# Performance work log

Hardware: AMD Instinct MI355X
Metric: run time of the kernel (lower is better)

## Reference

```python
import jax, jax.numpy as jnp
import numpy as np

T, B, K = 512, 512, 8
V, H, NL, NLAB = 5, 30, 4, 3


def setup_inputs() -> dict:
    key = jax.random.key(0)
    ks = jax.random.split(key, 12)
    s = 0.1
    return {
        "x": jax.random.randint(ks[0], (T, B, K), 0, V),
        "weight_of_x": jax.random.uniform(ks[1], (T, B, K), dtype=jnp.float32),
        "embed": jax.random.normal(ks[2], (V, H), dtype=jnp.float32) * s,
        "lstm_Wih": jax.random.normal(ks[3], (NL, 4 * H, H), dtype=jnp.float32) * s,
        "lstm_Whh": jax.random.normal(ks[4], (NL, 4 * H, H), dtype=jnp.float32) * s,
        "lstm_bih": jax.random.normal(ks[5], (NL, 4 * H), dtype=jnp.float32) * s,
        "lstm_bhh": jax.random.normal(ks[6], (NL, 4 * H), dtype=jnp.float32) * s,
        "attn_W1": jax.random.normal(ks[7], (H, 64), dtype=jnp.float32) * s,
        "attn_b1": jnp.zeros((64,), jnp.float32),
        "attn_W2": jax.random.normal(ks[8], (64, 1), dtype=jnp.float32) * s,
        "attn_b2": jnp.zeros((1,), jnp.float32),
        "fc_W": jax.random.normal(ks[9], (H, NLAB), dtype=jnp.float32) * s,
        "fc_b": jnp.zeros((NLAB,), jnp.float32),
    }


def _lstm_layer(xs, Wih, Whh, bih, bhh):
    # xs: (T, B, H_in); PyTorch gate order i, f, g, o
    b = bih + bhh
    Bsz = xs.shape[1]
    h0 = jnp.zeros((Bsz, Whh.shape[1]), xs.dtype)

    def step(carry, xt):
        h, c = carry
        gates = xt @ Wih.T + h @ Whh.T + b  # (B, 4H)
        i, f, g, o = jnp.split(gates, 4, axis=-1)
        i, f, o = jax.nn.sigmoid(i), jax.nn.sigmoid(f), jax.nn.sigmoid(o)
        g = jnp.tanh(g)
        c = f * c + i * g
        h = o * jnp.tanh(c)
        return (h, c), h

    _, hs = jax.lax.scan(step, (h0, h0), xs)
    return hs  # (T, B, H)


def reference(x, weight_of_x, embed, lstm_Wih, lstm_Whh, lstm_bih, lstm_bhh,
              attn_W1, attn_b1, attn_W2, attn_b2, fc_W, fc_b):
    # embedding + weighted mean pooling over K
    e = embed[x] * weight_of_x[..., None]          # (T, B, K, H)
    e = jax.nn.relu(e)
    seq = jnp.mean(e, axis=2)                      # (T, B, H)

    # 4-layer LSTM (loop over fixed num_layers)
    out = seq
    for l in range(lstm_Wih.shape[0]):
        out = _lstm_layer(out, lstm_Wih[l], lstm_Whh[l], lstm_bih[l], lstm_bhh[l])

    # attention pooling over time
    enc = jnp.transpose(out, (1, 0, 2))            # (B, T, H)
    energy = jax.nn.relu(enc @ attn_W1 + attn_b1) @ attn_W2 + attn_b2  # (B, T, 1)
    weights = jax.nn.softmax(energy[..., 0], axis=1)  # (B, T)
    pooled = jnp.sum(enc * weights[..., None], axis=1)  # (B, H)

    # dropout is identity in eval mode
    logit = jax.nn.softmax(pooled @ fc_W + fc_b, axis=1)  # (B, 3)
    return logit
```

## Files before the change

### kernel.cpp

```cpp
#include <hip/hip_runtime.h>

#define TT 512
#define BB 512
#define KK 8
#define HH 30
#define GG 120
#define NLAYER 4

__device__ __forceinline__ float rcp_f(float x) { return __builtin_amdgcn_rcpf(x); }
__device__ __forceinline__ float rdlane_f(float v, int l) {
    return __int_as_float(__builtin_amdgcn_readlane(__float_as_int(v), l));
}
__device__ __forceinline__ float2 pk_fma_v(float2 a, float2 b, float2 c) {
    float2 d;
    asm("v_pk_fma_f32 %0, %1, %2, %3" : "=v"(d) : "v"(a), "v"(b), "v"(c));
    return d;
}
__device__ __forceinline__ float2 pk_fma_s(float2 a, float2 bs, float2 c) {
    float2 d;
    asm("v_pk_fma_f32 %0, %1, %2, %3" : "=v"(d) : "v"(a), "s"(bs), "v"(c));
    return d;
}
__device__ __forceinline__ float2 pk_add(float2 a, float2 b) {
    float2 d;
    asm("v_pk_add_f32 %0, %1, %2" : "=v"(d) : "v"(a), "v"(b));
    return d;
}
__device__ __forceinline__ float swap32_hi(float x) {
    float a = x, b = x;
    asm("v_permlane32_swap_b32 %0, %1" : "+v"(a), "+v"(b));
    return b;
}

__global__ __launch_bounds__(256) __attribute__((amdgpu_waves_per_eu(2, 2)))
void rnn_fused(
    const int*   __restrict__ xin,  const float* __restrict__ wxin,
    const float* __restrict__ embed,
    const float* __restrict__ Wih,  const float* __restrict__ Whh,
    const float* __restrict__ bih,  const float* __restrict__ bhh,
    const float* __restrict__ W1,   const float* __restrict__ b1,
    const float* __restrict__ W2,   const float* __restrict__ b2,
    const float* __restrict__ fcW,  const float* __restrict__ fcb,
    float* __restrict__ out)
{
    __shared__ alignas(16) float hstore[TT * HH];
    __shared__ alignas(16) float seqring[2][16][32];
    __shared__ alignas(16) int   ringx[4][16][KK];
    __shared__ alignas(16) float ringw[4][16][KK];
    __shared__ alignas(16) float hring[3][16][32];
    __shared__ alignas(16) float re_s[5 * HH];
    __shared__ alignas(16) float energy_s[TT];
    __shared__ float red_s[16];
    __shared__ float part_s[8][HH];
    __shared__ float pooled_s[HH];
    __shared__ float logits_s[3];
    __shared__ int   sync_s[8];

    const int tid  = threadIdx.x;
    const int wv   = tid >> 6;
    const int lane = tid & 63;
    const int b    = blockIdx.x;
    volatile int* vs = sync_s;

    if (tid < 8) sync_s[tid] = 0;
    if (tid < 5 * HH) re_s[tid] = fmaxf(embed[tid], 0.0f);

    int4 hx = {0,0,0,0}; float4 hw = {0,0,0,0};
    if (wv == 0 && lane < 32) {
        const int r = lane >> 1, hf = lane & 1;
        #pragma unroll
        for (int cc = 0; cc < 2; ++cc) {
            long off = ((long)(16 * cc + r) * BB + b) * KK + hf * 4;
            *(int4*)(&ringx[cc][r][hf * 4])   = *(const int4*)(xin  + off);
            *(float4*)(&ringw[cc][r][hf * 4]) = *(const float4*)(wxin + off);
        }
        long off2 = ((long)(32 + r) * BB + b) * KK + hf * 4;
        hx = *(const int4*)(xin  + off2);
        hw = *(const float4*)(wxin + off2);
    }

    const int half = lane >> 5;
    const int q31  = lane & 31;
    const int qq   = (q31 < HH) ? q31 : (HH - 1);
    const int rA   = qq + half * HH;
    const int rB   = rA + 60;
    float2 wihA[15], wihB[15], whhA[15], whhB[15];
    {
        const float* WihL = Wih + wv * GG * HH;
        const float* WhhL = Whh + wv * GG * HH;
        #pragma unroll
        for (int kk = 0; kk < 15; ++kk) {
            wihA[kk] = *(const float2*)(WihL + rA * HH + 2 * kk);
            wihB[kk] = *(const float2*)(WihL + rB * HH + 2 * kk);
            whhA[kk] = *(const float2*)(WhhL + rA * HH + 2 * kk);
            whhB[kk] = *(const float2*)(WhhL + rB * HH + 2 * kk);
        }
    }
    const float biasA = bih[wv * GG + rA] + bhh[wv * GG + rA];
    const float biasB = bih[wv * GG + rB] + bhh[wv * GG + rB];
    const float mBneg = (lane < 32) ? -2.0f : -1.0f;
    const float aB    = (lane < 32) ?  2.0f :  1.0f;
    const float dB    = (lane < 32) ? -1.0f :  0.0f;

    __syncthreads();

    float c_val = 0.0f;
    float hprev = 0.0f;

    auto do_step = [&](int t) {
        const float* xsrc = (wv == 0) ? &seqring[(t >> 4) & 1][t & 15][0]
                                      : &hring[wv - 1][t & 15][0];
        float2 xp[15];
        #pragma unroll
        for (int k = 0; k < 15; ++k) xp[k] = *(const float2*)(xsrc + 2 * k);

        float2 ahA = {0.f,0.f}, ahB = {0.f,0.f};
        float2 ahA2 = {0.f,0.f}, ahB2 = {0.f,0.f};
        #pragma unroll
        for (int k = 0; k < 8; ++k) {
            float2 hp;
            hp.x = rdlane_f(hprev, 2 * k);
            hp.y = rdlane_f(hprev, 2 * k + 1);
            ahA = pk_fma_s(whhA[k], hp, ahA);
            ahB = pk_fma_s(whhB[k], hp, ahB);
        }
        #pragma unroll
        for (int k = 8; k < 15; ++k) {
            float2 hp;
            hp.x = rdlane_f(hprev, 2 * k);
            hp.y = rdlane_f(hprev, 2 * k + 1);
            ahA2 = pk_fma_s(whhA[k], hp, ahA2);
            ahB2 = pk_fma_s(whhB[k], hp, ahB2);
        }
        float2 axA = {0.f,0.f}, axB = {0.f,0.f};
        #pragma unroll
        for (int k = 0; k < 15; ++k) {
            axA = pk_fma_v(wihA[k], xp[k], axA);
            axB = pk_fma_v(wihB[k], xp[k], axB);
        }
        const float2 s0 = pk_add(pk_add(axA, ahA), ahA2);
        const float2 s1 = pk_add(pk_add(axB, ahB), ahB2);
        const float gA = s0.x + s0.y + biasA;
        const float gB = s1.x + s1.y + biasB;
        const float actA = rcp_f(1.0f + __expf(-gA));
        const float sB   = rcp_f(1.0f + __expf(gB * mBneg));
        const float actB = fmaf(aB, sB, dB);
        const float fI = swap32_hi(actA);
        const float oI = swap32_hi(actB);
        c_val = fmaf(fI, c_val, actA * actB);
        const float tC = fmaf(2.0f, rcp_f(1.0f + __expf(-2.0f * c_val)), -1.0f);
        const float hv = oI * tC;
        hprev = hv;
        if (lane < HH) {
            if (wv < NLAYER - 1) hring[wv][t & 15][lane] = hv;
            else                 hstore[t * HH + lane]  = hv;
        }
    };

    for (int T0 = 0; T0 < TT; T0 += 8) {
        if (wv == 0) {
            if ((T0 & 15) == 0) {
                const int c = T0 >> 4;
                if (lane < 32) {
                    const int r = lane >> 1, hf = lane & 1;
                    if (c <= 29) {
                        const int sl = (c + 2) & 3;
                        *(int4*)(&ringx[sl][r][hf * 4])   = hx;
                        *(float4*)(&ringw[sl][r][hf * 4]) = hw;
                    }
                    if (c <= 28) {
                        long off = ((long)(16 * (c + 3) + r) * BB + b) * KK + hf * 4;
                        hx = *(const int4*)(xin  + off);
                        hw = *(const float4*)(wxin + off);
                    }
                }
                const int sl = c & 3, par = c & 1;
                #pragma unroll
                for (int rr = 0; rr < 8; ++rr) {
                    const int o = lane + rr * 64;
                    if (o < 480) {
                        const int tr = o / HH, j = o - tr * HH;
                        int4   xa = *(const int4*)(&ringx[sl][tr][0]);
                        int4   xb = *(const int4*)(&ringx[sl][tr][4]);
                        float4 wa = *(const float4*)(&ringw[sl][tr][0]);
                        float4 wb = *(const float4*)(&ringw[sl][tr][4]);
                        float acc = re_s[xa.x * HH + j] * wa.x;
                        acc = fmaf(re_s[xa.y * HH + j], wa.y, acc);
                        acc = fmaf(re_s[xa.z * HH + j], wa.z, acc);
                        acc = fmaf(re_s[xa.w * HH + j], wa.w, acc);
                        acc = fmaf(re_s[xb.x * HH + j], wb.x, acc);
                        acc = fmaf(re_s[xb.y * HH + j], wb.y, acc);
                        acc = fmaf(re_s[xb.z * HH + j], wb.z, acc);
                        acc = fmaf(re_s[xb.w * HH + j], wb.w, acc);
                        seqring[par][tr][j] = acc * 0.125f;
                    }
                }
                __threadfence_block();
            }
        } else {
            while (vs[wv - 1] < T0 + 8) __builtin_amdgcn_s_sleep(1);
        }
        if (wv < NLAYER - 1) {
            while (vs[4 + wv + 1] < T0 - 8) __builtin_amdgcn_s_sleep(1);
        }
        __threadfence_block();
        do_step(T0 + 0);
        do_step(T0 + 1);
        do_step(T0 + 2);
        do_step(T0 + 3);
        do_step(T0 + 4);
        do_step(T0 + 5);
        do_step(T0 + 6);
        do_step(T0 + 7);
        __threadfence_block();
        if (lane == 0) {
            if (wv < NLAYER - 1) vs[wv]     = T0 + 8;
            if (wv > 0)          vs[4 + wv] = T0 + 8;
        }
    }

    __syncthreads();

    {
        const float* W1p = W1;
        const float* b1p = b1;
        const float* W2p = W2;
        asm volatile("" : "+v"(W1p), "+v"(b1p), "+v"(W2p));

        float w1cx[15], w1cy[15];
        #pragma unroll
        for (int k = 0; k < 15; ++k) {
            w1cx[k] = W1p[(2 * k) * 64 + lane];
            w1cy[k] = W1p[(2 * k + 1) * 64 + lane];
        }
        const float b1v = b1p[lane];
        const float w2v = W2p[lane];
        const float b2v = b2[0];
        #pragma unroll
        for (int pass = 0; pass < 2; ++pass) {
            const int t = wv * 128 + pass * 64 + lane;
            float2 h2[15];
            #pragma unroll
            for (int k = 0; k < 15; ++k)
                h2[k] = *(const float2*)(hstore + t * HH + 2 * k);
            float e = b2v;
            for (int u = 0; u < 64; ++u) {
                float2 acc = {0.f, 0.f};
                #pragma unroll
                for (int k = 0; k < 15; ++k) {
                    float2 wp;
                    wp.x = rdlane_f(w1cx[k], u);
                    wp.y = rdlane_f(w1cy[k], u);
                    acc = pk_fma_s(h2[k], wp, acc);
                }
                const float su = acc.x + acc.y + rdlane_f(b1v, u);
                e = fmaf(fmaxf(su, 0.0f), rdlane_f(w2v, u), e);
            }
            energy_s[t] = e;
        }
    }
    __syncthreads();

    float mx = -3.0e38f;
    for (int i = tid; i < TT; i += 256) mx = fmaxf(mx, energy_s[i]);
    #pragma unroll
    for (int m = 1; m < 64; m <<= 1) mx = fmaxf(mx, __shfl_xor(mx, m, 64));
    if (lane == 0) red_s[wv] = mx;
    __syncthreads();
    mx = fmaxf(fmaxf(red_s[0], red_s[1]), fmaxf(red_s[2], red_s[3]));
    float ssum = 0.0f;
    for (int i = tid; i < TT; i += 256) {
        float ev = __expf(energy_s[i] - mx);
        energy_s[i] = ev;
        ssum += ev;
    }
    #pragma unroll
    for (int m = 1; m < 64; m <<= 1) ssum += __shfl_xor(ssum, m, 64);
    if (lane == 0) red_s[8 + wv] = ssum;
    __syncthreads();
    const float invS = rcp_f(red_s[8] + red_s[9] + red_s[10] + red_s[11]);

    {
        const int g = tid >> 5, jj = tid & 31;
        if (jj < HH) {
            float part = 0.0f;
            for (int t = g; t < TT; t += 8)
                part = fmaf(energy_s[t] * invS, hstore[t * HH + jj], part);
            part_s[g][jj] = part;
        }
    }
    __syncthreads();
    if (tid < HH) {
        float pv = 0.0f;
        #pragma unroll
        for (int q = 0; q < 8; ++q) pv += part_s[q][tid];
        pooled_s[tid] = pv;
    }
    __syncthreads();

    if (tid < 3) {
        float acc = fcb[tid];
        #pragma unroll
        for (int k = 0; k < HH; ++k) acc = fmaf(pooled_s[k], fcW[k * 3 + tid], acc);
        logits_s[tid] = acc;
    }
    __syncthreads();
    if (tid == 0) {
        float l0 = logits_s[0], l1 = logits_s[1], l2 = logits_s[2];
        float m3 = fmaxf(l0, fmaxf(l1, l2));
        float e0 = __expf(l0 - m3), e1 = __expf(l1 - m3), e2 = __expf(l2 - m3);
        float inv = rcp_f(e0 + e1 + e2);
        out[b * 3 + 0] = e0 * inv; out[b * 3 + 1] = e1 * inv; out[b * 3 + 2] = e2 * inv;
    }
}

extern "C" void kernel_launch(void* const* d_in, const int* in_sizes, int n_in,
                              void* d_out, int out_size, void* d_ws, size_t ws_size,
                              hipStream_t stream)
{
    (void)in_sizes; (void)n_in; (void)d_ws; (void)ws_size; (void)out_size;
    rnn_fused<<<BB, 256, 0, stream>>>(
        (const int*)  d_in[0],  (const float*)d_in[1],  (const float*)d_in[2],
        (const float*)d_in[3],  (const float*)d_in[4],  (const float*)d_in[5],
        (const float*)d_in[6],  (const float*)d_in[7],  (const float*)d_in[8],
        (const float*)d_in[9],  (const float*)d_in[10], (const float*)d_in[11],
        (const float*)d_in[12], (float*)d_out);
}
```

Before: 452.8 us.

## Use fp16 weights and activations with fdot2 in LSTM recurrence

Converts the LSTM input and recurrent weights to packed fp16 and accumulates the gate dot products with v_dot2 fp16 instructions into fp32. Inter-layer hidden states and the embedded sequence are stored as packed half2 in shared memory, and adjacent lanes' h values are combined with a DPP swap so one readlane fetches two h values. This halves the register footprint and the readlane count on the serial per-step critical path. It also stops unrolling the 8-step loop. The cost is fp16 rounding of weights and activations across 512 recurrent steps and 4 layers, which may exceed the accuracy tolerance.

```diff
diff --git a/kernel.cpp b/kernel.cpp
--- a/kernel.cpp
+++ b/kernel.cpp
@@ -7,23 +7,21 @@
 #define GG 120
 #define NLAYER 4
 
+typedef _Float16 half2v __attribute__((ext_vector_type(2)));
+
 __device__ __forceinline__ float rcp_f(float x) { return __builtin_amdgcn_rcpf(x); }
 __device__ __forceinline__ float rdlane_f(float v, int l) {
     return __int_as_float(__builtin_amdgcn_readlane(__float_as_int(v), l));
 }
-__device__ __forceinline__ float2 pk_fma_v(float2 a, float2 b, float2 c) {
-    float2 d;
-    asm("v_pk_fma_f32 %0, %1, %2, %3" : "=v"(d) : "v"(a), "v"(b), "v"(c));
-    return d;
+__device__ __forceinline__ unsigned int rdlane_u(unsigned int v, int l) {
+    return (unsigned int)__builtin_amdgcn_readlane((int)v, l);
+}
+__device__ __forceinline__ half2v as_h2(unsigned int u) {
+    union { unsigned int u; half2v h; } c; c.u = u; return c.h;
 }
 __device__ __forceinline__ float2 pk_fma_s(float2 a, float2 bs, float2 c) {
     float2 d;
     asm("v_pk_fma_f32 %0, %1, %2, %3" : "=v"(d) : "v"(a), "s"(bs), "v"(c));
-    return d;
-}
-__device__ __forceinline__ float2 pk_add(float2 a, float2 b) {
-    float2 d;
-    asm("v_pk_add_f32 %0, %1, %2" : "=v"(d) : "v"(a), "v"(b));
     return d;
 }
 __device__ __forceinline__ float swap32_hi(float x) {
@@ -44,10 +42,10 @@
     float* __restrict__ out)
 {
     __shared__ alignas(16) float hstore[TT * HH];
-    __shared__ alignas(16) float seqring[2][16][32];
+    __shared__ alignas(16) unsigned int seqring16[2][16][16];
     __shared__ alignas(16) int   ringx[4][16][KK];
     __shared__ alignas(16) float ringw[4][16][KK];
-    __shared__ alignas(16) float hring[3][16][32];
+    __shared__ alignas(16) unsigned int hring16[3][16][16];
     __shared__ alignas(16) float re_s[5 * HH];
     __shared__ alignas(16) float energy_s[TT];
     __shared__ float red_s[16];
@@ -84,16 +82,20 @@
     const int qq   = (q31 < HH) ? q31 : (HH - 1);
     const int rA   = qq + half * HH;
     const int rB   = rA + 60;
-    float2 wihA[15], wihB[15], whhA[15], whhB[15];
+    half2v wihA_h[15], wihB_h[15], whhA_h[15], whhB_h[15];
     {
         const float* WihL = Wih + wv * GG * HH;
         const float* WhhL = Whh + wv * GG * HH;
         #pragma unroll
         for (int kk = 0; kk < 15; ++kk) {
-            wihA[kk] = *(const float2*)(WihL + rA * HH + 2 * kk);
-            wihB[kk] = *(const float2*)(WihL + rB * HH + 2 * kk);
-            whhA[kk] = *(const float2*)(WhhL + rA * HH + 2 * kk);
-            whhB[kk] = *(const float2*)(WhhL + rB * HH + 2 * kk);
+            float2 a0 = *(const float2*)(WihL + rA * HH + 2 * kk);
+            float2 a1 = *(const float2*)(WihL + rB * HH + 2 * kk);
+            float2 a2 = *(const float2*)(WhhL + rA * HH + 2 * kk);
+            float2 a3 = *(const float2*)(WhhL + rB * HH + 2 * kk);
+            wihA_h[kk][0] = (_Float16)a0.x; wihA_h[kk][1] = (_Float16)a0.y;
+            wihB_h[kk][0] = (_Float16)a1.x; wihB_h[kk][1] = (_Float16)a1.y;
+            whhA_h[kk][0] = (_Float16)a2.x; whhA_h[kk][1] = (_Float16)a2.y;
+            whhB_h[kk][0] = (_Float16)a3.x; whhB_h[kk][1] = (_Float16)a3.y;
         }
     }
     const float biasA = bih[wv * GG + rA] + bhh[wv * GG + rA];
@@ -105,43 +107,39 @@
     __syncthreads();
 
     float c_val = 0.0f;
-    float hprev = 0.0f;
+    unsigned int hpk = 0;
 
     auto do_step = [&](int t) {
-        const float* xsrc = (wv == 0) ? &seqring[(t >> 4) & 1][t & 15][0]
-                                      : &hring[wv - 1][t & 15][0];
-        float2 xp[15];
-        #pragma unroll
-        for (int k = 0; k < 15; ++k) xp[k] = *(const float2*)(xsrc + 2 * k);
-
-        float2 ahA = {0.f,0.f}, ahB = {0.f,0.f};
-        float2 ahA2 = {0.f,0.f}, ahB2 = {0.f,0.f};
+        const unsigned int* xsrc = (wv == 0) ? &seqring16[(t >> 4) & 1][t & 15][0]
+                                             : &hring16[wv - 1][t & 15][0];
+        uint4 q0 = ((const uint4*)xsrc)[0];
+        uint4 q1 = ((const uint4*)xsrc)[1];
+        uint4 q2 = ((const uint4*)xsrc)[2];
+        uint4 q3 = ((const uint4*)xsrc)[3];
+        const unsigned int xu[16] = {q0.x,q0.y,q0.z,q0.w, q1.x,q1.y,q1.z,q1.w,
+                                     q2.x,q2.y,q2.z,q2.w, q3.x,q3.y,q3.z,q3.w};
+        float ahA = 0.f, ahB = 0.f, ahA2 = 0.f, ahB2 = 0.f;
         #pragma unroll
         for (int k = 0; k < 8; ++k) {
-            float2 hp;
-            hp.x = rdlane_f(hprev, 2 * k);
-            hp.y = rdlane_f(hprev, 2 * k + 1);
-            ahA = pk_fma_s(whhA[k], hp, ahA);
-            ahB = pk_fma_s(whhB[k], hp, ahB);
+            const half2v hp = as_h2(rdlane_u(hpk, 2 * k));
+            ahA = __builtin_amdgcn_fdot2(whhA_h[k], hp, ahA, false);
+            ahB = __builtin_amdgcn_fdot2(whhB_h[k], hp, ahB, false);
         }
         #pragma unroll
         for (int k = 8; k < 15; ++k) {
-            float2 hp;
-            hp.x = rdlane_f(hprev, 2 * k);
-            hp.y = rdlane_f(hprev, 2 * k + 1);
-            ahA2 = pk_fma_s(whhA[k], hp, ahA2);
-            ahB2 = pk_fma_s(whhB[k], hp, ahB2);
-        }
-        float2 axA = {0.f,0.f}, axB = {0.f,0.f};
+            const half2v hp = as_h2(rdlane_u(hpk, 2 * k));
+            ahA2 = __builtin_amdgcn_fdot2(whhA_h[k], hp, ahA2, false);
+            ahB2 = __builtin_amdgcn_fdot2(whhB_h[k], hp, ahB2, false);
+        }
+        float axA = 0.f, axB = 0.f;
         #pragma unroll
         for (int k = 0; k < 15; ++k) {
-            axA = pk_fma_v(wihA[k], xp[k], axA);
-            axB = pk_fma_v(wihB[k], xp[k], axB);
-        }
-        const float2 s0 = pk_add(pk_add(axA, ahA), ahA2);
-        const float2 s1 = pk_add(pk_add(axB, ahB), ahB2);
-        const float gA = s0.x + s0.y + biasA;
-        const float gB = s1.x + s1.y + biasB;
+            const half2v xp = as_h2(xu[k]);
+            axA = __builtin_amdgcn_fdot2(wihA_h[k], xp, axA, false);
+            axB = __builtin_amdgcn_fdot2(wihB_h[k], xp, axB, false);
+        }
+        const float gA = (axA + ahA) + (ahA2 + biasA);
+        const float gB = (axB + ahB) + (ahB2 + biasB);
         const float actA = rcp_f(1.0f + __expf(-gA));
         const float sB   = rcp_f(1.0f + __expf(gB * mBneg));
         const float actB = fmaf(aB, sB, dB);
@@ -150,10 +148,15 @@
         c_val = fmaf(fI, c_val, actA * actB);
         const float tC = fmaf(2.0f, rcp_f(1.0f + __expf(-2.0f * c_val)), -1.0f);
         const float hv = oI * tC;
-        hprev = hv;
+        union { _Float16 f[2]; unsigned int u; } cv; cv.u = 0;
+        cv.f[0] = (_Float16)hv;
+        const unsigned int hu  = cv.u;
+        const unsigned int hup = (unsigned int)__builtin_amdgcn_mov_dpp(
+                                     (int)hu, 0xB1, 0xF, 0xF, true);
+        hpk = hu | (hup << 16);
         if (lane < HH) {
-            if (wv < NLAYER - 1) hring[wv][t & 15][lane] = hv;
-            else                 hstore[t * HH + lane]  = hv;
+            if (wv == NLAYER - 1) hstore[t * HH + lane] = hv;
+            else if (!(lane & 1)) hring16[wv][t & 15][lane >> 1] = hpk;
         }
     };
 
@@ -192,7 +195,7 @@
                         acc = fmaf(re_s[xb.y * HH + j], wb.y, acc);
                         acc = fmaf(re_s[xb.z * HH + j], wb.z, acc);
                         acc = fmaf(re_s[xb.w * HH + j], wb.w, acc);
-                        seqring[par][tr][j] = acc * 0.125f;
+                        ((_Float16*)&seqring16[par][tr][0])[j] = (_Float16)(acc * 0.125f);
                     }
                 }
                 __threadfence_block();
@@ -204,14 +207,9 @@
             while (vs[4 + wv + 1] < T0 - 8) __builtin_amdgcn_s_sleep(1);
         }
         __threadfence_block();
-        do_step(T0 + 0);
-        do_step(T0 + 1);
-        do_step(T0 + 2);
-        do_step(T0 + 3);
-        do_step(T0 + 4);
-        do_step(T0 + 5);
-        do_step(T0 + 6);
-        do_step(T0 + 7);
+        #pragma unroll 1
+        for (int tt = 0; tt < 8; ++tt)
+            do_step(T0 + tt);
         __threadfence_block();
         if (lane == 0) {
             if (wv < NLAYER - 1) vs[wv]     = T0 + 8;
```

Result: faster. 442.5 us (median of 2 runs) (-2.3%).
